# Kernel tuning notes

Hardware: AMD Instinct MI355X
Metric: run time of the kernel (lower is better)

Reference implementation:

```python
import jax, jax.numpy as jnp
import numpy as np

TEMPERATURE = 8.0  # sqrt(head_dim=64)
NEG_BIG = -10000.0


def setup_inputs() -> dict:
    key = jax.random.key(0)
    kq, kk, kv, km = jax.random.split(key, 4)
    B, H, S, D, K = 4, 8, 1024, 64, 4
    q = jax.random.normal(kq, (B, H, S, D), dtype=jnp.float32)
    k = jax.random.normal(kk, (B, H, S, D), dtype=jnp.float32)
    v = jax.random.normal(kv, (B, H, S, D), dtype=jnp.float32)
    # K binary attention masks, broadcastable to [B,H,S,S]
    mask = jax.random.randint(km, (K, 1, 1, S, S), 0, 2).astype(jnp.float32)
    return {"q": q, "k": k, "v": v, "mask": mask}


def reference(q, k, v, mask):
    # attn: [B,H,S,S]
    attn = jnp.einsum("bhsd,bhtd->bhst", q / TEMPERATURE, k)
    # additive mask: [K,1,1,S,S]
    ext_mask = (1.0 - mask) * NEG_BIG
    # batched over K instead of the original python loop: [K,B,H,S,S]
    probs = jax.nn.softmax(attn[None] + ext_mask, axis=-1)
    # dropout is identity in eval mode (deterministic reference)
    output = jnp.einsum("kbhst,bhtd->kbhsd", probs, v)
    return (output, attn)
```

## Files before the change

kernel.cpp:

```cpp
#include <hip/hip_runtime.h>
#include <hip/hip_bf16.h>
#include <stdint.h>

typedef float f4 __attribute__((ext_vector_type(4)));
typedef short bf8 __attribute__((ext_vector_type(8)));
typedef uint32_t u4 __attribute__((ext_vector_type(4)));
typedef uint32_t u2 __attribute__((ext_vector_type(2)));

#define SDIM 1024
#define DDIM 64
#define NBH  32
#define KM   4
#define NT   16

#define MB_BLK 4096
#define KB_BLK 1024
#define VT_BLK 512

__device__ __forceinline__ unsigned short f2bf(float f) {
  uint32_t u = __builtin_bit_cast(uint32_t, f);
  u += 0x7fffu + ((u >> 16) & 1u);
  return (unsigned short)(u >> 16);
}

#define GLOAD16(gsrc, ldst)                                                  \
  __builtin_amdgcn_global_load_lds(                                          \
      (const __attribute__((address_space(1))) unsigned int*)(gsrc),         \
      (__attribute__((address_space(3))) unsigned int*)(ldst), 16, 0, 0)

__device__ __forceinline__ bf8 lds_ld(const unsigned short* base, int row, int e0) {
  return *(const bf8*)((const char*)base + (((row * 64 + e0) * 2) ^ ((row & 7) << 4)));
}

__global__ __launch_bounds__(256) void prepass(
    const float* __restrict__ k, const float* __restrict__ v,
    const float* __restrict__ mask, unsigned short* __restrict__ kb,
    unsigned short* __restrict__ vt, uint32_t* __restrict__ mb2) {
  __shared__ float tv[64][65];
  const int b = blockIdx.x;
  const int t = threadIdx.x;
  if (b < MB_BLK) {
    int gid4 = (b * 256 + t) * 4;
    f4 x = *(const f4*)(mask + gid4);
    uint32_t bits = (x[0] > 0.5f ? 1u : 0u) | (x[1] > 0.5f ? 2u : 0u) |
                    (x[2] > 0.5f ? 4u : 0u) | (x[3] > 0.5f ? 8u : 0u);
    uint32_t wv = bits << (gid4 & 28);
    wv |= __shfl_xor(wv, 1);
    wv |= __shfl_xor(wv, 2);
    wv |= __shfl_xor(wv, 4);
    if ((t & 7) == 0) {
      int m = gid4 >> 20;
      int r = (gid4 >> 10) & 1023;
      int c = gid4 & 1023;
      mb2[m * 32768 + (c >> 5) * 1024 + r] = wv;
    }
  } else if (b < MB_BLK + KB_BLK) {
    int base = ((b - MB_BLK) * 256 + t) * 8;
    f4 a = *(const f4*)(k + base);
    f4 c = *(const f4*)(k + base + 4);
    bf8 o;
    o[0] = (short)f2bf(a[0]); o[1] = (short)f2bf(a[1]);
    o[2] = (short)f2bf(a[2]); o[3] = (short)f2bf(a[3]);
    o[4] = (short)f2bf(c[0]); o[5] = (short)f2bf(c[1]);
    o[6] = (short)f2bf(c[2]); o[7] = (short)f2bf(c[3]);
    *(bf8*)(kb + base) = o;
  } else {
    int vb = b - MB_BLK - KB_BLK;
    int bh = vb >> 4;
    int s0 = (vb & 15) * 64;
    int sr = t >> 2, c0 = (t & 3) * 16;
    const float* vp = v + ((size_t)(bh * SDIM) + s0 + sr) * DDIM + c0;
#pragma unroll
    for (int i = 0; i < 4; ++i) {
      f4 x = *(const f4*)(vp + 4 * i);
#pragma unroll
      for (int j = 0; j < 4; ++j) tv[sr][c0 + 4 * i + j] = x[j];
    }
    __syncthreads();
    int d = t >> 2, sc0 = (t & 3) * 16;
    unsigned short tmp[16];
#pragma unroll
    for (int i = 0; i < 16; ++i) tmp[i] = f2bf(tv[sc0 + i][d]);
    unsigned short* op = vt + ((size_t)(bh * DDIM) + d) * SDIM + s0 + sc0;
    bf8 o0, o1;
#pragma unroll
    for (int j = 0; j < 8; ++j) { o0[j] = (short)tmp[j]; o1[j] = (short)tmp[j + 8]; }
    *(bf8*)(op) = o0;
    *(bf8*)(op + 8) = o1;
  }
}

__global__ __launch_bounds__(512, 4) void attn_main(
    const float* __restrict__ qf, const unsigned short* __restrict__ kb,
    const unsigned short* __restrict__ vtg, const uint32_t* __restrict__ mb2,
    float* __restrict__ outO, float* __restrict__ attn) {
  __shared__ __align__(16) unsigned short k_s0[64 * 64];
  __shared__ __align__(16) unsigned short k_s1[64 * 64];
  __shared__ __align__(16) unsigned short v_s0[64 * 64];
  __shared__ __align__(16) unsigned short v_s1[64 * 64];
  __shared__ __align__(16) unsigned short e_s0[64 * 64];
  __shared__ __align__(16) unsigned short e_s1[64 * 64];

  const int tid = threadIdx.x;
  const int l   = tid & 63;
  const int w   = tid >> 6;
  const int l16 = l & 15;
  const int lg  = l >> 4;
  const int rt  = w >> 1;
  const int cp  = w & 1;

  int bid = (int)blockIdx.x;
  bid = (bid & 7) * 64 + (bid >> 3);
  const int bh = bid >> 4;
  const int r0 = (bid & 15) * 64;

  const int srow = tid >> 3;
  const int sd   = ((tid & 7) ^ (srow & 7)) << 3;
  const unsigned short* ksrc = kb  + ((size_t)(bh * SDIM) + srow) * DDIM + sd;
  const unsigned short* vsrc = vtg + ((size_t)(bh * DDIM) + srow) * SDIM + sd;

  GLOAD16(ksrc,        k_s0 + tid * 8);
  GLOAD16(ksrc + 4096, k_s1 + tid * 8);
  GLOAD16(vsrc,        v_s0 + tid * 8);

  bf8 bq0, bq1;
  {
    const float* qp = qf + ((size_t)(bh * SDIM) + r0 + 16 * rt + l16) * DDIM + lg * 8;
    f4 a0 = *(const f4*)qp;
    f4 a1 = *(const f4*)(qp + 4);
    f4 a2 = *(const f4*)(qp + 32);
    f4 a3 = *(const f4*)(qp + 36);
#pragma unroll
    for (int j = 0; j < 4; ++j) {
      bq0[j]     = (short)f2bf(a0[j] * 0.125f);
      bq0[j + 4] = (short)f2bf(a1[j] * 0.125f);
      bq1[j]     = (short)f2bf(a2[j] * 0.125f);
      bq1[j + 4] = (short)f2bf(a3[j] * 0.125f);
    }
  }

  f4 acc[2][4] = {};
  f4 accl[2]   = {};
  bf8 ones;
#pragma unroll
  for (int b = 0; b < 8; ++b) ones[b] = (short)0x3F80;

  const uint32_t* mbase = mb2 + rt * 32768 + r0 + l16;

  uint32_t mdwA[2][2], mdwB[2][2];
#pragma unroll
  for (int mt2 = 0; mt2 < 2; ++mt2)
#pragma unroll
    for (int kt = 0; kt < 2; ++kt)
      mdwA[mt2][kt] = mbase[kt * 1024 + 32 * cp + 16 * mt2];

  __syncthreads();

#define QKSTEP(CT, KN, EN)                                                     \
  {                                                                            \
    const int kc0 = 32 * cp + l16;                                             \
    bf8 ak0 = lds_ld((KN), kc0, lg * 8);                                       \
    bf8 ak1 = lds_ld((KN), kc0, lg * 8 + 32);                                  \
    bf8 ak2 = lds_ld((KN), kc0 + 16, lg * 8);                                  \
    bf8 ak3 = lds_ld((KN), kc0 + 16, lg * 8 + 32);                             \
    f4 s0 = {}, s1 = {};                                                       \
    s0 = __builtin_amdgcn_mfma_f32_16x16x32_bf16(ak0, bq0, s0, 0, 0, 0);       \
    s0 = __builtin_amdgcn_mfma_f32_16x16x32_bf16(ak1, bq1, s0, 0, 0, 0);       \
    s1 = __builtin_amdgcn_mfma_f32_16x16x32_bf16(ak2, bq0, s1, 0, 0, 0);       \
    s1 = __builtin_amdgcn_mfma_f32_16x16x32_bf16(ak3, bq1, s1, 0, 0, 0);       \
    float* arow = attn + ((size_t)(bh * SDIM) + r0 + 16 * rt + l16) * SDIM     \
                  + (CT) * 64 + 32 * cp + 4 * lg;                              \
    *(f4*)(arow) = s0;                                                         \
    *(f4*)(arow + 16) = s1;                                                    \
    const int erow = 16 * rt + l16;                                            \
    u2 ev0, ev1;                                                               \
    ev0[0] = (uint32_t)f2bf(__expf(s0[0])) | ((uint32_t)f2bf(__expf(s0[1])) << 16); \
    ev0[1] = (uint32_t)f2bf(__expf(s0[2])) | ((uint32_t)f2bf(__expf(s0[3])) << 16); \
    ev1[0] = (uint32_t)f2bf(__expf(s1[0])) | ((uint32_t)f2bf(__expf(s1[1])) << 16); \
    ev1[1] = (uint32_t)f2bf(__expf(s1[2])) | ((uint32_t)f2bf(__expf(s1[3])) << 16); \
    const int colA = 32 * cp + 4 * lg;                                         \
    *(u2*)((char*)(EN) + (((erow * 64 + colA) * 2) ^ ((erow & 7) << 4))) = ev0; \
    *(u2*)((char*)(EN) + (((erow * 64 + colA + 16) * 2) ^ ((erow & 7) << 4))) = ev1; \
  }

  QKSTEP(0, k_s0, e_s0)
  asm volatile("s_waitcnt lgkmcnt(0)\n\ts_barrier" ::: "memory");

#define BODY(CT, KN, VC, KW, VW, EC, EN, MC, MN, QKF, PFK, PFV)                \
  {                                                                            \
    if (PFK) GLOAD16(ksrc + (size_t)((CT) + 2) * 4096, (KW) + tid * 8);        \
    if (PFV) GLOAD16(vsrc + (size_t)((CT) + 1) * 64, (VW) + tid * 8);          \
    if (QKF) QKSTEP((CT) + 1, KN, EN)                                          \
    {                                                                          \
      bf8 af[2][2];                                                            \
      _Pragma("unroll") for (int mt2 = 0; mt2 < 2; ++mt2) {                    \
        const int row = 32 * cp + 16 * mt2 + l16;                              \
        _Pragma("unroll") for (int kt = 0; kt < 2; ++kt) {                     \
          bf8 e = lds_ld((EC), row, kt * 32 + lg * 8);                         \
          uint32_t bits = ((MC)[mt2][kt] >> (lg * 8)) & 0xffu;                 \
          u4 ew = __builtin_bit_cast(u4, e);                                   \
          _Pragma("unroll") for (int d = 0; d < 4; ++d) {                      \
            uint32_t n2 = (bits >> (2 * d)) & 3u;                              \
            uint32_t sp = (n2 * 0x8001u) & 0x00010001u;                        \
            ew[d] &= (sp << 16) - sp;                                          \
          }                                                                    \
          af[mt2][kt] = __builtin_bit_cast(bf8, ew);                           \
        }                                                                      \
        accl[mt2] = __builtin_amdgcn_mfma_f32_16x16x32_bf16(af[mt2][0], ones, accl[mt2], 0, 0, 0); \
        accl[mt2] = __builtin_amdgcn_mfma_f32_16x16x32_bf16(af[mt2][1], ones, accl[mt2], 0, 0, 0); \
      }                                                                        \
      _Pragma("unroll") for (int nt = 0; nt < 4; ++nt) {                       \
        const int dc = 16 * nt + l16;                                          \
        bf8 bv0 = lds_ld((VC), dc, lg * 8);                                    \
        bf8 bv1 = lds_ld((VC), dc, lg * 8 + 32);                               \
        _Pragma("unroll") for (int mt2 = 0; mt2 < 2; ++mt2) {                  \
          acc[mt2][nt] = __builtin_amdgcn_mfma_f32_16x16x32_bf16(af[mt2][0], bv0, acc[mt2][nt], 0, 0, 0); \
          acc[mt2][nt] = __builtin_amdgcn_mfma_f32_16x16x32_bf16(af[mt2][1], bv1, acc[mt2][nt], 0, 0, 0); \
        }                                                                      \
      }                                                                        \
    }                                                                          \
    if (QKF) {                                                                 \
      _Pragma("unroll") for (int mt2 = 0; mt2 < 2; ++mt2)                      \
        _Pragma("unroll") for (int kt = 0; kt < 2; ++kt)                       \
          (MN)[mt2][kt] = mbase[(((CT) + 1) * 2 + kt) * 1024 + 32 * cp + 16 * mt2]; \
    }                                                                          \
    __syncthreads();                                                           \
  }

  for (int ct2 = 0; ct2 < NT / 2; ++ct2) {
    const bool lastp = (ct2 == NT / 2 - 1);
    BODY(2 * ct2,     k_s1, v_s0, k_s0, v_s1, e_s0, e_s1, mdwA, mdwB,
         true, !lastp, true)
    BODY(2 * ct2 + 1, k_s0, v_s1, k_s1, v_s0, e_s1, e_s0, mdwB, mdwA,
         !lastp, !lastp, !lastp)
  }
#undef BODY
#undef QKSTEP

#pragma unroll
  for (int mt2 = 0; mt2 < 2; ++mt2) {
#pragma unroll
    for (int r = 0; r < 4; ++r) {
      float inv = 1.0f / accl[mt2][r];
      int row = 32 * cp + 16 * mt2 + 4 * lg + r;
      float* orow = outO + (((size_t)(rt * NBH + bh)) * SDIM + r0 + row) * DDIM + l16;
#pragma unroll
      for (int nt = 0; nt < 4; ++nt)
        orow[16 * nt] = acc[mt2][nt][r] * inv;
    }
  }
}

extern "C" void kernel_launch(void* const* d_in, const int* in_sizes, int n_in,
                              void* d_out, int out_size, void* d_ws, size_t ws_size,
                              hipStream_t stream) {
  (void)in_sizes; (void)n_in; (void)out_size; (void)ws_size;
  const float* q    = (const float*)d_in[0];
  const float* k    = (const float*)d_in[1];
  const float* v    = (const float*)d_in[2];
  const float* mask = (const float*)d_in[3];
  float* outO = (float*)d_out;
  float* attn = (float*)d_out + (size_t)KM * NBH * SDIM * DDIM;

  char* ws = (char*)d_ws;
  unsigned short* kb = (unsigned short*)ws;
  unsigned short* vt = (unsigned short*)(ws + (4u << 20));
  uint32_t*       mb = (uint32_t*)(ws + (8u << 20));

  prepass<<<MB_BLK + KB_BLK + VT_BLK, 256, 0, stream>>>(k, v, mask, kb, vt, mb);
  attn_main<<<NBH * 16, 512, 0, stream>>>(q, kb, vt, mb, outO, attn);
}
```

Measured before the change: 53.47 us.

## Halve query tile to 32 rows and use 256-thread blocks

Each block now handles 32 query rows instead of 64, using 4 waves instead of 8, and the grid doubles to 1024 blocks. Each wave now owns one mask index k (all four k's per block) rather than splitting columns, and the exp tile in LDS shrinks accordingly. This gives more blocks to spread across CUs and cuts LDS per block. In exchange, K and V tiles are loaded twice as often per query row, and each thread issues two global-to-LDS loads per tile.

```diff
diff --git a/kernel.cpp b/kernel.cpp
--- a/kernel.cpp
+++ b/kernel.cpp
@@ -90,7 +90,7 @@
   }
 }
 
-__global__ __launch_bounds__(512, 4) void attn_main(
+__global__ __launch_bounds__(256, 4) void attn_main(
     const float* __restrict__ qf, const unsigned short* __restrict__ kb,
     const unsigned short* __restrict__ vtg, const uint32_t* __restrict__ mb2,
     float* __restrict__ outO, float* __restrict__ attn) {
@@ -98,34 +98,39 @@
   __shared__ __align__(16) unsigned short k_s1[64 * 64];
   __shared__ __align__(16) unsigned short v_s0[64 * 64];
   __shared__ __align__(16) unsigned short v_s1[64 * 64];
-  __shared__ __align__(16) unsigned short e_s0[64 * 64];
-  __shared__ __align__(16) unsigned short e_s1[64 * 64];
+  __shared__ __align__(16) unsigned short e_s0[32 * 64];
+  __shared__ __align__(16) unsigned short e_s1[32 * 64];
 
   const int tid = threadIdx.x;
   const int l   = tid & 63;
   const int w   = tid >> 6;
   const int l16 = l & 15;
   const int lg  = l >> 4;
-  const int rt  = w >> 1;
-  const int cp  = w & 1;
+  const int wh  = w & 1;
+  const int wc  = w >> 1;
 
   int bid = (int)blockIdx.x;
-  bid = (bid & 7) * 64 + (bid >> 3);
-  const int bh = bid >> 4;
-  const int r0 = (bid & 15) * 64;
+  bid = (bid & 7) * 128 + (bid >> 3);
+  const int bh = bid >> 5;
+  const int r0 = (bid & 31) * 32;
 
   const int srow = tid >> 3;
   const int sd   = ((tid & 7) ^ (srow & 7)) << 3;
-  const unsigned short* ksrc = kb  + ((size_t)(bh * SDIM) + srow) * DDIM + sd;
-  const unsigned short* vsrc = vtg + ((size_t)(bh * DDIM) + srow) * SDIM + sd;
-
-  GLOAD16(ksrc,        k_s0 + tid * 8);
-  GLOAD16(ksrc + 4096, k_s1 + tid * 8);
-  GLOAD16(vsrc,        v_s0 + tid * 8);
+  const unsigned short* ksrc0 = kb  + ((size_t)(bh * SDIM) + srow) * DDIM + sd;
+  const unsigned short* ksrc1 = kb  + ((size_t)(bh * SDIM) + srow + 32) * DDIM + sd;
+  const unsigned short* vsrc0 = vtg + ((size_t)(bh * DDIM) + srow) * SDIM + sd;
+  const unsigned short* vsrc1 = vtg + ((size_t)(bh * DDIM) + srow + 32) * SDIM + sd;
+
+  GLOAD16(ksrc0,        k_s0 + tid * 8);
+  GLOAD16(ksrc1,        k_s0 + (tid + 256) * 8);
+  GLOAD16(ksrc0 + 4096, k_s1 + tid * 8);
+  GLOAD16(ksrc1 + 4096, k_s1 + (tid + 256) * 8);
+  GLOAD16(vsrc0,        v_s0 + tid * 8);
+  GLOAD16(vsrc1,        v_s0 + (tid + 256) * 8);
 
   bf8 bq0, bq1;
   {
-    const float* qp = qf + ((size_t)(bh * SDIM) + r0 + 16 * rt + l16) * DDIM + lg * 8;
+    const float* qp = qf + ((size_t)(bh * SDIM) + r0 + 16 * wh + l16) * DDIM + lg * 8;
     f4 a0 = *(const f4*)qp;
     f4 a1 = *(const f4*)(qp + 4);
     f4 a2 = *(const f4*)(qp + 32);
@@ -145,20 +150,20 @@
 #pragma unroll
   for (int b = 0; b < 8; ++b) ones[b] = (short)0x3F80;
 
-  const uint32_t* mbase = mb2 + rt * 32768 + r0 + l16;
+  const uint32_t* mbase = mb2 + w * 32768 + r0 + l16;
 
   uint32_t mdwA[2][2], mdwB[2][2];
 #pragma unroll
   for (int mt2 = 0; mt2 < 2; ++mt2)
 #pragma unroll
     for (int kt = 0; kt < 2; ++kt)
-      mdwA[mt2][kt] = mbase[kt * 1024 + 32 * cp + 16 * mt2];
+      mdwA[mt2][kt] = mbase[kt * 1024 + 16 * mt2];
 
   __syncthreads();
 
 #define QKSTEP(CT, KN, EN)                                                     \
   {                                                                            \
-    const int kc0 = 32 * cp + l16;                                             \
+    const int kc0 = 32 * wc + l16;                                             \
     bf8 ak0 = lds_ld((KN), kc0, lg * 8);                                       \
     bf8 ak1 = lds_ld((KN), kc0, lg * 8 + 32);                                  \
     bf8 ak2 = lds_ld((KN), kc0 + 16, lg * 8);                                  \
@@ -168,17 +173,17 @@
     s0 = __builtin_amdgcn_mfma_f32_16x16x32_bf16(ak1, bq1, s0, 0, 0, 0);       \
     s1 = __builtin_amdgcn_mfma_f32_16x16x32_bf16(ak2, bq0, s1, 0, 0, 0);       \
     s1 = __builtin_amdgcn_mfma_f32_16x16x32_bf16(ak3, bq1, s1, 0, 0, 0);       \
-    float* arow = attn + ((size_t)(bh * SDIM) + r0 + 16 * rt + l16) * SDIM     \
-                  + (CT) * 64 + 32 * cp + 4 * lg;                              \
+    float* arow = attn + ((size_t)(bh * SDIM) + r0 + 16 * wh + l16) * SDIM     \
+                  + (CT) * 64 + 32 * wc + 4 * lg;                              \
     *(f4*)(arow) = s0;                                                         \
     *(f4*)(arow + 16) = s1;                                                    \
-    const int erow = 16 * rt + l16;                                            \
+    const int erow = 16 * wh + l16;                                            \
     u2 ev0, ev1;                                                               \
     ev0[0] = (uint32_t)f2bf(__expf(s0[0])) | ((uint32_t)f2bf(__expf(s0[1])) << 16); \
     ev0[1] = (uint32_t)f2bf(__expf(s0[2])) | ((uint32_t)f2bf(__expf(s0[3])) << 16); \
     ev1[0] = (uint32_t)f2bf(__expf(s1[0])) | ((uint32_t)f2bf(__expf(s1[1])) << 16); \
     ev1[1] = (uint32_t)f2bf(__expf(s1[2])) | ((uint32_t)f2bf(__expf(s1[3])) << 16); \
-    const int colA = 32 * cp + 4 * lg;                                         \
+    const int colA = 32 * wc + 4 * lg;                                         \
     *(u2*)((char*)(EN) + (((erow * 64 + colA) * 2) ^ ((erow & 7) << 4))) = ev0; \
     *(u2*)((char*)(EN) + (((erow * 64 + colA + 16) * 2) ^ ((erow & 7) << 4))) = ev1; \
   }
@@ -188,13 +193,19 @@
 
 #define BODY(CT, KN, VC, KW, VW, EC, EN, MC, MN, QKF, PFK, PFV)                \
   {                                                                            \
-    if (PFK) GLOAD16(ksrc + (size_t)((CT) + 2) * 4096, (KW) + tid * 8);        \
-    if (PFV) GLOAD16(vsrc + (size_t)((CT) + 1) * 64, (VW) + tid * 8);          \
+    if (PFK) {                                                                 \
+      GLOAD16(ksrc0 + (size_t)((CT) + 2) * 4096, (KW) + tid * 8);              \
+      GLOAD16(ksrc1 + (size_t)((CT) + 2) * 4096, (KW) + (tid + 256) * 8);      \
+    }                                                                          \
+    if (PFV) {                                                                 \
+      GLOAD16(vsrc0 + (size_t)((CT) + 1) * 64, (VW) + tid * 8);                \
+      GLOAD16(vsrc1 + (size_t)((CT) + 1) * 64, (VW) + (tid + 256) * 8);        \
+    }                                                                          \
     if (QKF) QKSTEP((CT) + 1, KN, EN)                                          \
     {                                                                          \
       bf8 af[2][2];                                                            \
       _Pragma("unroll") for (int mt2 = 0; mt2 < 2; ++mt2) {                    \
-        const int row = 32 * cp + 16 * mt2 + l16;                              \
+        const int row = 16 * mt2 + l16;                                        \
         _Pragma("unroll") for (int kt = 0; kt < 2; ++kt) {                     \
           bf8 e = lds_ld((EC), row, kt * 32 + lg * 8);                         \
           uint32_t bits = ((MC)[mt2][kt] >> (lg * 8)) & 0xffu;                 \
@@ -222,7 +233,7 @@
     if (QKF) {                                                                 \
       _Pragma("unroll") for (int mt2 = 0; mt2 < 2; ++mt2)                      \
         _Pragma("unroll") for (int kt = 0; kt < 2; ++kt)                       \
-          (MN)[mt2][kt] = mbase[(((CT) + 1) * 2 + kt) * 1024 + 32 * cp + 16 * mt2]; \
+          (MN)[mt2][kt] = mbase[(((CT) + 1) * 2 + kt) * 1024 + 16 * mt2];      \
     }                                                                          \
     __syncthreads();                                                           \
   }
@@ -242,8 +253,8 @@
 #pragma unroll
     for (int r = 0; r < 4; ++r) {
       float inv = 1.0f / accl[mt2][r];
-      int row = 32 * cp + 16 * mt2 + 4 * lg + r;
-      float* orow = outO + (((size_t)(rt * NBH + bh)) * SDIM + r0 + row) * DDIM + l16;
+      int row = 16 * mt2 + 4 * lg + r;
+      float* orow = outO + (((size_t)(w * NBH + bh)) * SDIM + r0 + row) * DDIM + l16;
 #pragma unroll
       for (int nt = 0; nt < 4; ++nt)
         orow[16 * nt] = acc[mt2][nt][r] * inv;
@@ -268,5 +279,5 @@
   uint32_t*       mb = (uint32_t*)(ws + (8u << 20));
 
   prepass<<<MB_BLK + KB_BLK + VT_BLK, 256, 0, stream>>>(k, v, mask, kb, vt, mb);
-  attn_main<<<NBH * 16, 512, 0, stream>>>(q, kb, vt, mb, outO, attn);
-}
+  attn_main<<<NBH * 32, 256, 0, stream>>>(q, kb, vt, mb, outO, attn);
+}
```

New measurement: 54.05 us. Within noise of the previous version (+1.1%).
